# Kernel tuning notes

Hardware: AMD Instinct MI355X
Metric: run time of the kernel (lower is better)

The kernel has to match this reference:

```python
import jax, jax.numpy as jnp
import numpy as np

MAX_OBJECTS = 20
NODE_FEAT_DIM = 16
HID = 256
N_OPS = 8
N_COLORS = 10
B = 16384
EPS = 1e-5


def _ln(x, g, b):
    m = x.mean(-1, keepdims=True)
    v = ((x - m) ** 2).mean(-1, keepdims=True)
    return (x - m) / jnp.sqrt(v + EPS) * g + b


def _mlp(x, w1, b1, w2, b2):
    return jax.nn.relu(x @ w1 + b1) @ w2 + b2


def setup_inputs() -> dict:
    key = jax.random.key(0)
    ks = jax.random.split(key, 32)
    w = lambda k, shp: (jax.random.normal(k, shp, jnp.float32) * 0.02)
    return {
        "nf": jax.random.normal(ks[0], (B, MAX_OBJECTS, NODE_FEAT_DIM), jnp.float32),
        "nn_c": jax.random.randint(ks[1], (B,), 0, MAX_OBJECTS),
        "neW": w(ks[2], (NODE_FEAT_DIM, HID)), "neb": jnp.zeros((HID,), jnp.float32),
        "g1W1": w(ks[3], (2 * HID, HID)), "g1b1": jnp.zeros((HID,), jnp.float32),
        "g1W2": w(ks[4], (HID, HID)), "g1b2": jnp.zeros((HID,), jnp.float32),
        "g2W1": w(ks[5], (2 * HID, HID)), "g2b1": jnp.zeros((HID,), jnp.float32),
        "g2W2": w(ks[6], (HID, HID)), "g2b2": jnp.zeros((HID,), jnp.float32),
        "n1g": jnp.ones((HID,), jnp.float32), "n1b": jnp.zeros((HID,), jnp.float32),
        "n2g": jnp.ones((HID,), jnp.float32), "n2b": jnp.zeros((HID,), jnp.float32),
        "ohW": w(ks[7], (HID, N_OPS)), "ohb": jnp.zeros((N_OPS,), jnp.float32),
        "c1W": w(ks[8], (HID, N_COLORS)), "c1b": jnp.zeros((N_COLORS,), jnp.float32),
        "c2W": w(ks[9], (HID, N_COLORS)), "c2b": jnp.zeros((N_COLORS,), jnp.float32),
        "pqW": w(ks[10], (HID, HID)), "pqb": jnp.zeros((HID,), jnp.float32),
        "pkW": w(ks[11], (HID, HID)), "pkb": jnp.zeros((HID,), jnp.float32),
    }


def reference(nf, nn_c, neW, neb, g1W1, g1b1, g1W2, g1b2, g2W1, g2b1, g2W2, g2b2,
              n1g, n1b, n2g, n2b, ohW, ohb, c1W, c1b, c2W, c2b, pqW, pqb, pkW, pkb):
    mask = jnp.arange(MAX_OBJECTS)[None, :] < nn_c[:, None]  # [B, N]
    mf = mask.astype(jnp.float32)[..., None]                 # [B, N, 1]
    denom = jnp.clip(mf.sum(1, keepdims=True), 1.0)          # [B, 1, 1]

    h = nf @ neW + neb                                       # [B, N, H]
    msg = (h * mf).sum(1, keepdims=True) / denom             # [B, 1, H]
    h = h + _mlp(jnp.concatenate([h, jnp.broadcast_to(msg, h.shape)], -1), g1W1, g1b1, g1W2, g1b2)
    h = _ln(h, n1g, n1b) * mf

    msg = (h * mf).sum(1, keepdims=True) / denom
    h = h + _mlp(jnp.concatenate([h, jnp.broadcast_to(msg, h.shape)], -1), g2W1, g2b1, g2W2, g2b2)
    h = _ln(h, n2g, n2b) * mf

    g = (h * mf).sum(1) / jnp.clip(mf.sum(1), 1.0)           # [B, H]

    q = g @ pqW + pqb                                        # [B, H]
    k = h @ pkW + pkb                                        # [B, N, H]
    pl = jnp.einsum('bh,bnh->bn', q, k)
    pl = jnp.where(mask, pl, -1e9)
    return (g @ ohW + ohb, g @ c1W + c1b, g @ c2W + c2b, pl)
```

## Files before the change

kernel.cpp:

```cpp
#include <hip/hip_runtime.h>

typedef unsigned char u8;
typedef unsigned int  u32;
using f32x4 = __attribute__((ext_vector_type(4))) float;

#define DI __device__ __forceinline__

DI u32 pk4f8(float a, float b, float c, float d){
  int w = __builtin_amdgcn_cvt_pk_fp8_f32(a, b, 0, false);
  w = __builtin_amdgcn_cvt_pk_fp8_f32(c, d, w, true);
  return (u32)w;
}
DI u8 enc1(float a){
  return (u8)(__builtin_amdgcn_cvt_pk_fp8_f32(a, a, 0, false) & 0xFF);
}
DI float dc0(u32 v){ return __builtin_amdgcn_cvt_f32_fp8((int)v, 0); }
DI float dc1(u32 v){ return __builtin_amdgcn_cvt_f32_fp8((int)v, 1); }
DI float dc2(u32 v){ return __builtin_amdgcn_cvt_f32_fp8((int)v, 2); }
DI float dc3(u32 v){ return __builtin_amdgcn_cvt_f32_fp8((int)v, 3); }

DI f32x4 MFMA8(long a, long b, f32x4 c){
  return __builtin_amdgcn_mfma_f32_16x16x32_fp8_fp8(a, b, c, 0, 0, 0);
}

DI int swz8(int row, int col){ return (row << 8) + (col ^ ((row & 15) << 3)); }
DI long ldsA8(const u8* buf, int row, int k0){ return *(const long*)(buf + swz8(row, k0)); }
DI long ldG8(const u8* p){ return *(const long*)p; }

DI long mk8(float v0, float v1, float v2, float v3, float v4, float v5, float v6, float v7){
  u32 lo = pk4f8(v0, v1, v2, v3), hi = pk4f8(v4, v5, v6, v7);
  return (long)(((unsigned long long)hi << 32) | (unsigned long long)lo);
}
DI long loadW8T(const float* __restrict__ W, int n, int k0){
  return mk8(W[(k0+0)*256+n]*8.f, W[(k0+1)*256+n]*8.f, W[(k0+2)*256+n]*8.f, W[(k0+3)*256+n]*8.f,
             W[(k0+4)*256+n]*8.f, W[(k0+5)*256+n]*8.f, W[(k0+6)*256+n]*8.f, W[(k0+7)*256+n]*8.f);
}
DI long loadW8T16(const float* __restrict__ W, int n, int k0){
  float v[8];
#pragma unroll
  for (int j = 0; j < 8; j++){ int k = k0 + j; v[j] = (k < 16) ? W[k*256+n]*8.f : 0.f; }
  return mk8(v[0],v[1],v[2],v[3],v[4],v[5],v[6],v[7]);
}
DI long loadW8row(const float* __restrict__ W, int n, int k0){
  const float* p = W + n*256 + k0;
  return mk8(p[0]*8.f,p[1]*8.f,p[2]*8.f,p[3]*8.f,p[4]*8.f,p[5]*8.f,p[6]*8.f,p[7]*8.f);
}

#define WS_NEWT  0
#define WS_W1AT1 8192
#define WS_W1BT1 73728
#define WS_W2T1  139264
#define WS_W1AT2 204800
#define WS_W1BT2 270336
#define WS_W2T2  335872
#define WS_PQWT  401408
#define WS_PKWP  466944
#define WS_TOTAL 532480

__global__ void prep_weights(
    const float* __restrict__ neW, const float* __restrict__ g1W1,
    const float* __restrict__ g1W2, const float* __restrict__ g2W1,
    const float* __restrict__ g2W2, const float* __restrict__ pqW,
    const float* __restrict__ pkW, u8* __restrict__ ws)
{
  int i = blockIdx.x * 256 + threadIdx.x;
  if (i >= WS_TOTAL) return;
  float v;
  if (i < 8192){
    int n = i >> 5, k = i & 31;
    v = (k < 16) ? neW[k * 256 + n] : 0.0f;
  } else {
    int j = i - 8192;
    int region = j >> 16;
    int idx = j & 65535;
    int n = idx >> 8, k = idx & 255;
    switch (region){
      case 0: v = g1W1[k * 256 + n]; break;
      case 1: v = g1W1[(256 + k) * 256 + n]; break;
      case 2: v = g1W2[k * 256 + n]; break;
      case 3: v = g2W1[k * 256 + n]; break;
      case 4: v = g2W1[(256 + k) * 256 + n]; break;
      case 5: v = g2W2[k * 256 + n]; break;
      case 6: v = pqW[k * 256 + n]; break;
      default: v = pkW[idx]; break;
    }
  }
  ws[i] = enc1(v * 8.0f);
}

template<bool PREPPED>
__global__ __launch_bounds__(512, 2) void fused_graphnet(
    const float* __restrict__ nf, const int* __restrict__ nn_c,
    const float* __restrict__ neW, const float* __restrict__ neb,
    const float* __restrict__ g1W1, const float* __restrict__ g1b1,
    const float* __restrict__ g1W2, const float* __restrict__ g1b2,
    const float* __restrict__ g2W1, const float* __restrict__ g2b1,
    const float* __restrict__ g2W2, const float* __restrict__ g2b2,
    const float* __restrict__ n1g, const float* __restrict__ n1b,
    const float* __restrict__ n2g, const float* __restrict__ n2b,
    const float* __restrict__ ohW, const float* __restrict__ ohb,
    const float* __restrict__ c1W, const float* __restrict__ c1b,
    const float* __restrict__ c2W, const float* __restrict__ c2b,
    const float* __restrict__ pqW, const float* __restrict__ pqb,
    const float* __restrict__ pkW, const float* __restrict__ pkb,
    const u8* __restrict__ ws, float* __restrict__ out,
    int out_n, int Bv)
{
  __shared__ __align__(16) u8 bufA[80 * 256];
  __shared__ __align__(16) u8 bufB[80 * 256];
  __shared__ __align__(16) u8 smallA[8 * 256];
  __shared__ float pbf[4 * 256];
  __shared__ float rowstats[8][80][2];
  __shared__ float qdot[4];
  __shared__ int   cntS[4];
  __shared__ float dinvS[4];

  const int b0 = blockIdx.x * 4;
  const int tid = threadIdx.x;
  const int wave = tid >> 6, lane = tid & 63;
  const int lg = lane >> 4, lc = lane & 15;
  const int n0 = wave * 32;

  const int Bout = out_n / 48;
  const int off_c1 = 8 * Bout;
  const int off_c2 = 18 * Bout;
  const int off_pl = 28 * Bout;

  if (tid < 4){
    int bi = b0 + tid; if (bi >= Bv) bi = Bv - 1;
    int c = nn_c[bi];
    c = c < 0 ? 0 : (c > 20 ? 20 : c);
    cntS[tid] = c;
    dinvS[tid] = 1.0f / (float)(c < 1 ? 1 : c);
  }

  for (int i = tid; i < 80 * 4; i += 512){
    int row = i >> 2, c0 = 16 + (i & 3) * 4;
    *(u32*)(bufB + swz8(row, c0)) = 0u;
  }
  for (int i = tid; i < 80 * 4; i += 512){
    int row = i >> 2, k0 = (i & 3) * 4;
    int gr = b0 * 20 + row; if (gr >= Bv * 20) gr = Bv * 20 - 1;
    const float* p = nf + gr * 16 + k0;
    *(u32*)(bufB + swz8(row, k0)) = pk4f8(p[0], p[1], p[2], p[3]);
  }
  __syncthreads();

  const f32x4 zero4 = {0.0f, 0.0f, 0.0f, 0.0f};

  {
    long bw0, bw1;
    if constexpr (PREPPED){
      bw0 = ldG8(ws + WS_NEWT + (n0 + lc) * 32 + lg * 8);
      bw1 = ldG8(ws + WS_NEWT + (n0 + 16 + lc) * 32 + lg * 8);
    } else {
      bw0 = loadW8T16(neW, n0 + lc, lg * 8);
      bw1 = loadW8T16(neW, n0 + 16 + lc, lg * 8);
    }
    f32x4 acc[5][2];
#pragma unroll
    for (int mt = 0; mt < 5; mt++){
      long a = ldsA8(bufB, mt * 16 + lc, lg * 8);
      acc[mt][0] = MFMA8(a, bw0, zero4);
      acc[mt][1] = MFMA8(a, bw1, zero4);
    }
#pragma unroll
    for (int nt = 0; nt < 2; nt++){
      float bb = neb[n0 + nt * 16 + lc];
#pragma unroll
      for (int mt = 0; mt < 5; mt++)
#pragma unroll
        for (int r = 0; r < 4; r++){
          int row = mt * 16 + lg * 4 + r;
          int col = n0 + nt * 16 + lc;
          bufA[swz8(row, col)] = enc1(acc[mt][nt][r] * 0.125f + bb);
        }
    }
  }
  __syncthreads();

  for (int rd = 0; rd < 2; rd++){
    const int w1at = (rd == 0) ? WS_W1AT1 : WS_W1AT2;
    const int w1bt = (rd == 0) ? WS_W1BT1 : WS_W1BT2;
    const int w2t  = (rd == 0) ? WS_W2T1  : WS_W2T2;
    const float* W1 = (rd == 0) ? g1W1 : g2W1;
    const float* W2 = (rd == 0) ? g1W2 : g2W2;
    const float* b1p = (rd == 0) ? g1b1 : g2b1;
    const float* b2p = (rd == 0) ? g1b2 : g2b2;
    const float* ngp = (rd == 0) ? n1g : n2g;
    const float* nbp = (rd == 0) ? n1b : n2b;

    if (tid < 256){
      int b = tid >> 6;
      int c0 = (tid & 63) * 4;
      int c = cntS[b];
      float s0 = 0, s1 = 0, s2 = 0, s3 = 0;
      for (int r = 0; r < c; r++){
        u32 v = *(const u32*)(bufA + swz8(b * 20 + r, c0));
        s0 += dc0(v); s1 += dc1(v); s2 += dc2(v); s3 += dc3(v);
      }
      float di = dinvS[b];
      *(u32*)(smallA + swz8(b, c0)) = pk4f8(s0 * di, s1 * di, s2 * di, s3 * di);
    }
    __syncthreads();

    {
      long bw[16];
#pragma unroll
      for (int kk = 0; kk < 8; kk++){
        if constexpr (PREPPED){
          bw[kk * 2 + 0] = ldG8(ws + w1bt + (n0 + lc) * 256 + kk * 32 + lg * 8);
          bw[kk * 2 + 1] = ldG8(ws + w1bt + (n0 + 16 + lc) * 256 + kk * 32 + lg * 8);
        } else {
          bw[kk * 2 + 0] = loadW8T(W1 + 256 * 256, n0 + lc, kk * 32 + lg * 8);
          bw[kk * 2 + 1] = loadW8T(W1 + 256 * 256, n0 + 16 + lc, kk * 32 + lg * 8);
        }
      }
      f32x4 acc0 = zero4, acc1 = zero4;
#pragma unroll
      for (int kk = 0; kk < 8; kk++){
        long a = ldsA8(smallA, lc & 3, kk * 32 + lg * 8);
        acc0 = MFMA8(a, bw[kk * 2 + 0], acc0);
        acc1 = MFMA8(a, bw[kk * 2 + 1], acc1);
      }
      if (lg == 0){
#pragma unroll
        for (int r = 0; r < 4; r++){
          pbf[r * 256 + (n0 + lc)]      = acc0[r] * 0.125f + b1p[n0 + lc];
          pbf[r * 256 + (n0 + 16 + lc)] = acc1[r] * 0.125f + b1p[n0 + 16 + lc];
        }
      }
    }

    {
      long bw[16];
#pragma unroll
      for (int kk = 0; kk < 8; kk++){
        if constexpr (PREPPED){
          bw[kk * 2 + 0] = ldG8(ws + w1at + (n0 + lc) * 256 + kk * 32 + lg * 8);
          bw[kk * 2 + 1] = ldG8(ws + w1at + (n0 + 16 + lc) * 256 + kk * 32 + lg * 8);
        } else {
          bw[kk * 2 + 0] = loadW8T(W1, n0 + lc, kk * 32 + lg * 8);
          bw[kk * 2 + 1] = loadW8T(W1, n0 + 16 + lc, kk * 32 + lg * 8);
        }
      }
      f32x4 tacc[5][2];
#pragma unroll
      for (int mt = 0; mt < 5; mt++)
#pragma unroll
        for (int nt = 0; nt < 2; nt++) tacc[mt][nt] = zero4;
#pragma unroll
      for (int kk = 0; kk < 8; kk++){
#pragma unroll
        for (int mt = 0; mt < 5; mt++){
          long a = ldsA8(bufA, mt * 16 + lc, kk * 32 + lg * 8);
          tacc[mt][0] = MFMA8(a, bw[kk * 2 + 0], tacc[mt][0]);
          tacc[mt][1] = MFMA8(a, bw[kk * 2 + 1], tacc[mt][1]);
        }
      }
#pragma unroll
      for (int mt = 0; mt < 5; mt++)
#pragma unroll
        for (int nt = 0; nt < 2; nt++)
#pragma unroll
          for (int r = 0; r < 4; r++){
            int row = mt * 16 + lg * 4 + r;
            int col = n0 + nt * 16 + lc;
            float v = tacc[mt][nt][r] * 0.125f + pbf[(row / 20) * 256 + col];
            bufB[swz8(row, col)] = enc1(fmaxf(v, 0.0f));
          }
    }
    __syncthreads();

    {
      long bw[16];
#pragma unroll
      for (int kk = 0; kk < 8; kk++){
        if constexpr (PREPPED){
          bw[kk * 2 + 0] = ldG8(ws + w2t + (n0 + lc) * 256 + kk * 32 + lg * 8);
          bw[kk * 2 + 1] = ldG8(ws + w2t + (n0 + 16 + lc) * 256 + kk * 32 + lg * 8);
        } else {
          bw[kk * 2 + 0] = loadW8T(W2, n0 + lc, kk * 32 + lg * 8);
          bw[kk * 2 + 1] = loadW8T(W2, n0 + 16 + lc, kk * 32 + lg * 8);
        }
      }
      f32x4 tacc[5][2];
#pragma unroll
      for (int mt = 0; mt < 5; mt++)
#pragma unroll
        for (int nt = 0; nt < 2; nt++) tacc[mt][nt] = zero4;
#pragma unroll
      for (int kk = 0; kk < 8; kk++){
#pragma unroll
        for (int mt = 0; mt < 5; mt++){
          long a = ldsA8(bufB, mt * 16 + lc, kk * 32 + lg * 8);
          tacc[mt][0] = MFMA8(a, bw[kk * 2 + 0], tacc[mt][0]);
          tacc[mt][1] = MFMA8(a, bw[kk * 2 + 1], tacc[mt][1]);
        }
      }
#pragma unroll
      for (int nt = 0; nt < 2; nt++){
        float b2s = b2p[n0 + nt * 16 + lc];
#pragma unroll
        for (int mt = 0; mt < 5; mt++)
#pragma unroll
          for (int r = 0; r < 4; r++){
            int row = mt * 16 + lg * 4 + r;
            int col = n0 + nt * 16 + lc;
            u32 rv = bufA[swz8(row, col)];
            float v = tacc[mt][nt][r] * 0.125f + dc0(rv) + b2s;
            bufA[swz8(row, col)] = enc1(v);
          }
      }
    }

    {
#pragma unroll
      for (int mt = 0; mt < 5; mt++)
#pragma unroll
        for (int r = 0; r < 4; r++){
          int row = mt * 16 + lg * 4 + r;
          float s1 = 0, s2 = 0;
#pragma unroll
          for (int nt = 0; nt < 2; nt++){
            float v = dc0((u32)bufA[swz8(row, n0 + nt * 16 + lc)]);
            s1 += v; s2 += v * v;
          }
#pragma unroll
          for (int d = 1; d < 16; d <<= 1){ s1 += __shfl_xor(s1, d, 64); s2 += __shfl_xor(s2, d, 64); }
          if (lc == 0){ rowstats[wave][row][0] = s1; rowstats[wave][row][1] = s2; }
        }
      __syncthreads();

#pragma unroll
      for (int mt = 0; mt < 5; mt++)
#pragma unroll
        for (int r = 0; r < 4; r++){
          int row = mt * 16 + lg * 4 + r;
          float t1s = 0, t2s = 0;
#pragma unroll
          for (int w = 0; w < 8; w++){ t1s += rowstats[w][row][0]; t2s += rowstats[w][row][1]; }
          float mean = t1s * (1.0f / 256.0f);
          float var  = t2s * (1.0f / 256.0f) - mean * mean;
          float rstd = rsqrtf(fmaxf(var, 0.0f) + 1e-5f);
          int bb = row / 20;
          float mf = ((row - bb * 20) < cntS[bb]) ? 1.0f : 0.0f;
#pragma unroll
          for (int nt = 0; nt < 2; nt++){
            int col = n0 + nt * 16 + lc;
            float v = dc0((u32)bufA[swz8(row, col)]);
            bufA[swz8(row, col)] = enc1(((v - mean) * rstd * ngp[col] + nbp[col]) * mf);
          }
        }
    }
    __syncthreads();
  }

  if (tid < 256){
    int b = tid >> 6;
    int c0 = (tid & 63) * 4;
    int c = cntS[b];
    float s0 = 0, s1 = 0, s2 = 0, s3 = 0;
    for (int r = 0; r < c; r++){
      u32 v = *(const u32*)(bufA + swz8(b * 20 + r, c0));
      s0 += dc0(v); s1 += dc1(v); s2 += dc2(v); s3 += dc3(v);
    }
    float di = dinvS[b];
    *(u32*)(smallA + swz8(b, c0)) = pk4f8(s0 * di, s1 * di, s2 * di, s3 * di);
  }
  __syncthreads();

  {
    long bw[16];
#pragma unroll
    for (int kk = 0; kk < 8; kk++){
      if constexpr (PREPPED){
        bw[kk * 2 + 0] = ldG8(ws + WS_PQWT + (n0 + lc) * 256 + kk * 32 + lg * 8);
        bw[kk * 2 + 1] = ldG8(ws + WS_PQWT + (n0 + 16 + lc) * 256 + kk * 32 + lg * 8);
      } else {
        bw[kk * 2 + 0] = loadW8T(pqW, n0 + lc, kk * 32 + lg * 8);
        bw[kk * 2 + 1] = loadW8T(pqW, n0 + 16 + lc, kk * 32 + lg * 8);
      }
    }
    f32x4 qacc0 = zero4, qacc1 = zero4;
#pragma unroll
    for (int kk = 0; kk < 8; kk++){
      long a = ldsA8(smallA, lc & 3, kk * 32 + lg * 8);
      qacc0 = MFMA8(a, bw[kk * 2 + 0], qacc0);
      qacc1 = MFMA8(a, bw[kk * 2 + 1], qacc1);
    }
    if (lg == 0){
#pragma unroll
      for (int r = 0; r < 4; r++){
        smallA[swz8(4 + r, n0 + lc)]      = enc1(qacc0[r] * 0.125f + pqb[n0 + lc]);
        smallA[swz8(4 + r, n0 + 16 + lc)] = enc1(qacc1[r] * 0.125f + pqb[n0 + 16 + lc]);
      }
    }
  }
  __syncthreads();

  if (wave < 4){
    u32 qv = *(const u32*)(smallA + swz8(4 + wave, lane * 4));
    float p = dc0(qv) * pkb[lane * 4 + 0] + dc1(qv) * pkb[lane * 4 + 1]
            + dc2(qv) * pkb[lane * 4 + 2] + dc3(qv) * pkb[lane * 4 + 3];
#pragma unroll
    for (int d = 1; d < 64; d <<= 1) p += __shfl_xor(p, d, 64);
    if (lane == 0) qdot[wave] = p;
  }

  {
    long bw[16];
#pragma unroll
    for (int kk = 0; kk < 8; kk++){
      if constexpr (PREPPED){
        bw[kk * 2 + 0] = ldG8(ws + WS_PKWP + (n0 + lc) * 256 + kk * 32 + lg * 8);
        bw[kk * 2 + 1] = ldG8(ws + WS_PKWP + (n0 + 16 + lc) * 256 + kk * 32 + lg * 8);
      } else {
        bw[kk * 2 + 0] = loadW8row(pkW, n0 + lc, kk * 32 + lg * 8);
        bw[kk * 2 + 1] = loadW8row(pkW, n0 + 16 + lc, kk * 32 + lg * 8);
      }
    }
    f32x4 racc0 = zero4, racc1 = zero4;
#pragma unroll
    for (int kk = 0; kk < 8; kk++){
      long a = ldsA8(smallA, 4 + (lc & 3), kk * 32 + lg * 8);
      racc0 = MFMA8(a, bw[kk * 2 + 0], racc0);
      racc1 = MFMA8(a, bw[kk * 2 + 1], racc1);
    }
    if (lg == 0){
#pragma unroll
      for (int r = 0; r < 4; r++){
        pbf[r * 256 + (n0 + lc)]      = racc0[r] * 0.125f;
        pbf[r * 256 + (n0 + 16 + lc)] = racc1[r] * 0.125f;
      }
    }
  }
  __syncthreads();

  if (wave < 4){
    const int b = wave;
    if (b0 + b < Bv){
      int cb = cntS[b];
      float qd = qdot[b];
      for (int rr = 0; rr < 20; rr++){
        int row = b * 20 + rr;
        u32 hv = *(const u32*)(bufA + swz8(row, lane * 4));
        const float* rp = pbf + b * 256 + lane * 4;
        float p = dc0(hv) * rp[0] + dc1(hv) * rp[1] + dc2(hv) * rp[2] + dc3(hv) * rp[3];
#pragma unroll
        for (int d = 1; d < 64; d <<= 1) p += __shfl_xor(p, d, 64);
        if (lane == 0){
          float v = (rr < cb) ? (p + qd) : -1e9f;
          out[off_pl + (b0 + b) * 20 + rr] = v;
        }
      }
    }
  } else {
    const int b = wave - 4;
    if (b0 + b < Bv){
      u32 gv = *(const u32*)(smallA + swz8(b, lane * 4));
      float g0 = dc0(gv), g1 = dc1(gv), g2 = dc2(gv), g3 = dc3(gv);
#pragma unroll 1
      for (int o = 0; o < 28; o++){
        const float* W; const float* bias; int ncol, col, off;
        if (o < 8)      { W = ohW; bias = ohb; ncol = 8;  col = o;      off = 0; }
        else if (o < 18){ W = c1W; bias = c1b; ncol = 10; col = o - 8;  off = off_c1; }
        else            { W = c2W; bias = c2b; ncol = 10; col = o - 18; off = off_c2; }
        int k = lane * 4;
        float p = g0 * W[(k + 0) * ncol + col] + g1 * W[(k + 1) * ncol + col]
                + g2 * W[(k + 2) * ncol + col] + g3 * W[(k + 3) * ncol + col];
#pragma unroll
        for (int d = 1; d < 64; d <<= 1) p += __shfl_xor(p, d, 64);
        if (lane == 0) out[off + (b0 + b) * ncol + col] = p + bias[col];
      }
    }
  }
}

extern "C" void kernel_launch(void* const* d_in, const int* in_sizes, int n_in,
                              void* d_out, int out_size, void* d_ws, size_t ws_size,
                              hipStream_t stream)
{
  const float* nf   = (const float*)d_in[0];
  const int*   nn_c = (const int*)d_in[1];
  const float* neW  = (const float*)d_in[2];
  const float* neb  = (const float*)d_in[3];
  const float* g1W1 = (const float*)d_in[4];
  const float* g1b1 = (const float*)d_in[5];
  const float* g1W2 = (const float*)d_in[6];
  const float* g1b2 = (const float*)d_in[7];
  const float* g2W1 = (const float*)d_in[8];
  const float* g2b1 = (const float*)d_in[9];
  const float* g2W2 = (const float*)d_in[10];
  const float* g2b2 = (const float*)d_in[11];
  const float* n1g  = (const float*)d_in[12];
  const float* n1b  = (const float*)d_in[13];
  const float* n2g  = (const float*)d_in[14];
  const float* n2b  = (const float*)d_in[15];
  const float* ohW  = (const float*)d_in[16];
  const float* ohb  = (const float*)d_in[17];
  const float* c1W  = (const float*)d_in[18];
  const float* c1b  = (const float*)d_in[19];
  const float* c2W  = (const float*)d_in[20];
  const float* c2b  = (const float*)d_in[21];
  const float* pqW  = (const float*)d_in[22];
  const float* pqb  = (const float*)d_in[23];
  const float* pkW  = (const float*)d_in[24];
  const float* pkb  = (const float*)d_in[25];

  float* outp = (float*)d_out;
  u8* ws = (u8*)d_ws;
  int B = in_sizes[0] / 320;
  int grid = (B + 3) / 4;

  if (ws_size >= (size_t)WS_TOTAL){
    prep_weights<<<(WS_TOTAL + 255) / 256, 256, 0, stream>>>(
        neW, g1W1, g1W2, g2W1, g2W2, pqW, pkW, ws);
    fused_graphnet<true><<<grid, 512, 0, stream>>>(
        nf, nn_c, neW, neb, g1W1, g1b1, g1W2, g1b2, g2W1, g2b1, g2W2, g2b2,
        n1g, n1b, n2g, n2b, ohW, ohb, c1W, c1b, c2W, c2b, pqW, pqb, pkW, pkb,
        ws, outp, out_size, B);
  } else {
    fused_graphnet<false><<<grid, 512, 0, stream>>>(
        nf, nn_c, neW, neb, g1W1, g1b1, g1W2, g1b2, g2W1, g2b1, g2W2, g2b2,
        n1g, n1b, n2g, n2b, ohW, ohb, c1W, c1b, c2W, c2b, pqW, pqb, pkW, pkb,
        ws, outp, out_size, B);
  }
}
```

Before: 1.118 ms.

## Process eight graphs per 1024-thread block with two row halves sharing weight loads

```diff
diff --git a/kernel.cpp b/kernel.cpp
--- a/kernel.cpp
+++ b/kernel.cpp
@@ -89,7 +89,7 @@
 }
 
 template<bool PREPPED>
-__global__ __launch_bounds__(512, 2) void fused_graphnet(
+__global__ __launch_bounds__(1024, 2) void fused_graphnet(
     const float* __restrict__ nf, const int* __restrict__ nn_c,
     const float* __restrict__ neW, const float* __restrict__ neb,
     const float* __restrict__ g1W1, const float* __restrict__ g1b1,
@@ -106,27 +106,29 @@
     const u8* __restrict__ ws, float* __restrict__ out,
     int out_n, int Bv)
 {
-  __shared__ __align__(16) u8 bufA[80 * 256];
-  __shared__ __align__(16) u8 bufB[80 * 256];
-  __shared__ __align__(16) u8 smallA[8 * 256];
-  __shared__ float pbf[4 * 256];
-  __shared__ float rowstats[8][80][2];
-  __shared__ float qdot[4];
-  __shared__ int   cntS[4];
-  __shared__ float dinvS[4];
-
-  const int b0 = blockIdx.x * 4;
+  __shared__ __align__(16) u8 bufA[160 * 256];
+  __shared__ __align__(16) u8 bufB[160 * 256];
+  __shared__ __align__(16) u8 smallA[16 * 256];
+  __shared__ float pbf[8 * 256];
+  __shared__ float rowstats[8][160][2];
+  __shared__ float qdot[8];
+  __shared__ int   cntS[8];
+  __shared__ float dinvS[8];
+
+  const int b0 = blockIdx.x * 8;
   const int tid = threadIdx.x;
   const int wave = tid >> 6, lane = tid & 63;
   const int lg = lane >> 4, lc = lane & 15;
-  const int n0 = wave * 32;
+  const int rh = wave >> 3, cw = wave & 7;
+  const int n0 = cw * 32;
+  const int rb = rh * 80;
 
   const int Bout = out_n / 48;
   const int off_c1 = 8 * Bout;
   const int off_c2 = 18 * Bout;
   const int off_pl = 28 * Bout;
 
-  if (tid < 4){
+  if (tid < 8){
     int bi = b0 + tid; if (bi >= Bv) bi = Bv - 1;
     int c = nn_c[bi];
     c = c < 0 ? 0 : (c > 20 ? 20 : c);
@@ -134,12 +136,13 @@
     dinvS[tid] = 1.0f / (float)(c < 1 ? 1 : c);
   }
 
-  for (int i = tid; i < 80 * 4; i += 512){
-    int row = i >> 2, c0 = 16 + (i & 3) * 4;
+  if (tid < 16 * 64) *(u32*)(smallA + tid * 4) = 0u;
+  if (tid < 160 * 4){
+    int row = tid >> 2, c0 = 16 + (tid & 3) * 4;
     *(u32*)(bufB + swz8(row, c0)) = 0u;
   }
-  for (int i = tid; i < 80 * 4; i += 512){
-    int row = i >> 2, k0 = (i & 3) * 4;
+  if (tid < 160 * 4){
+    int row = tid >> 2, k0 = (tid & 3) * 4;
     int gr = b0 * 20 + row; if (gr >= Bv * 20) gr = Bv * 20 - 1;
     const float* p = nf + gr * 16 + k0;
     *(u32*)(bufB + swz8(row, k0)) = pk4f8(p[0], p[1], p[2], p[3]);
@@ -160,7 +163,7 @@
     f32x4 acc[5][2];
 #pragma unroll
     for (int mt = 0; mt < 5; mt++){
-      long a = ldsA8(bufB, mt * 16 + lc, lg * 8);
+      long a = ldsA8(bufB, rb + mt * 16 + lc, lg * 8);
       acc[mt][0] = MFMA8(a, bw0, zero4);
       acc[mt][1] = MFMA8(a, bw1, zero4);
     }
@@ -171,7 +174,7 @@
       for (int mt = 0; mt < 5; mt++)
 #pragma unroll
         for (int r = 0; r < 4; r++){
-          int row = mt * 16 + lg * 4 + r;
+          int row = rb + mt * 16 + lg * 4 + r;
           int col = n0 + nt * 16 + lc;
           bufA[swz8(row, col)] = enc1(acc[mt][nt][r] * 0.125f + bb);
         }
@@ -190,7 +193,7 @@
     const float* ngp = (rd == 0) ? n1g : n2g;
     const float* nbp = (rd == 0) ? n1b : n2b;
 
-    if (tid < 256){
+    if (tid < 512){
       int b = tid >> 6;
       int c0 = (tid & 63) * 4;
       int c = cntS[b];
@@ -219,15 +222,16 @@
       f32x4 acc0 = zero4, acc1 = zero4;
 #pragma unroll
       for (int kk = 0; kk < 8; kk++){
-        long a = ldsA8(smallA, lc & 3, kk * 32 + lg * 8);
+        long a = ldsA8(smallA, lc, kk * 32 + lg * 8);
         acc0 = MFMA8(a, bw[kk * 2 + 0], acc0);
         acc1 = MFMA8(a, bw[kk * 2 + 1], acc1);
       }
-      if (lg == 0){
+      if (rh == 0 && lg < 2){
 #pragma unroll
         for (int r = 0; r < 4; r++){
-          pbf[r * 256 + (n0 + lc)]      = acc0[r] * 0.125f + b1p[n0 + lc];
-          pbf[r * 256 + (n0 + 16 + lc)] = acc1[r] * 0.125f + b1p[n0 + 16 + lc];
+          int b = lg * 4 + r;
+          pbf[b * 256 + (n0 + lc)]      = acc0[r] * 0.125f + b1p[n0 + lc];
+          pbf[b * 256 + (n0 + 16 + lc)] = acc1[r] * 0.125f + b1p[n0 + 16 + lc];
         }
       }
     }
@@ -253,18 +257,19 @@
       for (int kk = 0; kk < 8; kk++){
 #pragma unroll
         for (int mt = 0; mt < 5; mt++){
-          long a = ldsA8(bufA, mt * 16 + lc, kk * 32 + lg * 8);
+          long a = ldsA8(bufA, rb + mt * 16 + lc, kk * 32 + lg * 8);
           tacc[mt][0] = MFMA8(a, bw[kk * 2 + 0], tacc[mt][0]);
           tacc[mt][1] = MFMA8(a, bw[kk * 2 + 1], tacc[mt][1]);
         }
       }
+      __syncthreads();
 #pragma unroll
       for (int mt = 0; mt < 5; mt++)
 #pragma unroll
         for (int nt = 0; nt < 2; nt++)
 #pragma unroll
           for (int r = 0; r < 4; r++){
-            int row = mt * 16 + lg * 4 + r;
+            int row = rb + mt * 16 + lg * 4 + r;
             int col = n0 + nt * 16 + lc;
             float v = tacc[mt][nt][r] * 0.125f + pbf[(row / 20) * 256 + col];
             bufB[swz8(row, col)] = enc1(fmaxf(v, 0.0f));
@@ -293,7 +298,7 @@
       for (int kk = 0; kk < 8; kk++){
 #pragma unroll
         for (int mt = 0; mt < 5; mt++){
-          long a = ldsA8(bufB, mt * 16 + lc, kk * 32 + lg * 8);
+          long a = ldsA8(bufB, rb + mt * 16 + lc, kk * 32 + lg * 8);
           tacc[mt][0] = MFMA8(a, bw[kk * 2 + 0], tacc[mt][0]);
           tacc[mt][1] = MFMA8(a, bw[kk * 2 + 1], tacc[mt][1]);
         }
@@ -305,7 +310,7 @@
         for (int mt = 0; mt < 5; mt++)
 #pragma unroll
           for (int r = 0; r < 4; r++){
-            int row = mt * 16 + lg * 4 + r;
+            int row = rb + mt * 16 + lg * 4 + r;
             int col = n0 + nt * 16 + lc;
             u32 rv = bufA[swz8(row, col)];
             float v = tacc[mt][nt][r] * 0.125f + dc0(rv) + b2s;
@@ -319,7 +324,7 @@
       for (int mt = 0; mt < 5; mt++)
 #pragma unroll
         for (int r = 0; r < 4; r++){
-          int row = mt * 16 + lg * 4 + r;
+          int row = rb + mt * 16 + lg * 4 + r;
           float s1 = 0, s2 = 0;
 #pragma unroll
           for (int nt = 0; nt < 2; nt++){
@@ -328,15 +333,21 @@
           }
 #pragma unroll
           for (int d = 1; d < 16; d <<= 1){ s1 += __shfl_xor(s1, d, 64); s2 += __shfl_xor(s2, d, 64); }
-          if (lc == 0){ rowstats[wave][row][0] = s1; rowstats[wave][row][1] = s2; }
+          if (lc == 0){ rowstats[cw][row][0] = s1; rowstats[cw][row][1] = s2; }
         }
       __syncthreads();
 
+      float ngv[2], nbv[2];
+#pragma unroll
+      for (int nt = 0; nt < 2; nt++){
+        ngv[nt] = ngp[n0 + nt * 16 + lc];
+        nbv[nt] = nbp[n0 + nt * 16 + lc];
+      }
 #pragma unroll
       for (int mt = 0; mt < 5; mt++)
 #pragma unroll
         for (int r = 0; r < 4; r++){
-          int row = mt * 16 + lg * 4 + r;
+          int row = rb + mt * 16 + lg * 4 + r;
           float t1s = 0, t2s = 0;
 #pragma unroll
           for (int w = 0; w < 8; w++){ t1s += rowstats[w][row][0]; t2s += rowstats[w][row][1]; }
@@ -349,14 +360,14 @@
           for (int nt = 0; nt < 2; nt++){
             int col = n0 + nt * 16 + lc;
             float v = dc0((u32)bufA[swz8(row, col)]);
-            bufA[swz8(row, col)] = enc1(((v - mean) * rstd * ngp[col] + nbp[col]) * mf);
+            bufA[swz8(row, col)] = enc1(((v - mean) * rstd * ngv[nt] + nbv[nt]) * mf);
           }
         }
     }
     __syncthreads();
   }
 
-  if (tid < 256){
+  if (tid < 512){
     int b = tid >> 6;
     int c0 = (tid & 63) * 4;
     int c = cntS[b];
@@ -385,22 +396,24 @@
     f32x4 qacc0 = zero4, qacc1 = zero4;
 #pragma unroll
     for (int kk = 0; kk < 8; kk++){
-      long a = ldsA8(smallA, lc & 3, kk * 32 + lg * 8);
+      long a = ldsA8(smallA, lc, kk * 32 + lg * 8);
       qacc0 = MFMA8(a, bw[kk * 2 + 0], qacc0);
       qacc1 = MFMA8(a, bw[kk * 2 + 1], qacc1);
     }
-    if (lg == 0){
+    __syncthreads();
+    if (rh == 0 && lg < 2){
 #pragma unroll
       for (int r = 0; r < 4; r++){
-        smallA[swz8(4 + r, n0 + lc)]      = enc1(qacc0[r] * 0.125f + pqb[n0 + lc]);
-        smallA[swz8(4 + r, n0 + 16 + lc)] = enc1(qacc1[r] * 0.125f + pqb[n0 + 16 + lc]);
+        int b = lg * 4 + r;
+        smallA[swz8(8 + b, n0 + lc)]      = enc1(qacc0[r] * 0.125f + pqb[n0 + lc]);
+        smallA[swz8(8 + b, n0 + 16 + lc)] = enc1(qacc1[r] * 0.125f + pqb[n0 + 16 + lc]);
       }
     }
   }
   __syncthreads();
 
-  if (wave < 4){
-    u32 qv = *(const u32*)(smallA + swz8(4 + wave, lane * 4));
+  if (wave < 8){
+    u32 qv = *(const u32*)(smallA + swz8(8 + wave, lane * 4));
     float p = dc0(qv) * pkb[lane * 4 + 0] + dc1(qv) * pkb[lane * 4 + 1]
             + dc2(qv) * pkb[lane * 4 + 2] + dc3(qv) * pkb[lane * 4 + 3];
 #pragma unroll
@@ -423,26 +436,28 @@
     f32x4 racc0 = zero4, racc1 = zero4;
 #pragma unroll
     for (int kk = 0; kk < 8; kk++){
-      long a = ldsA8(smallA, 4 + (lc & 3), kk * 32 + lg * 8);
+      long a = ldsA8(smallA, 8 + (lc & 7), kk * 32 + lg * 8);
       racc0 = MFMA8(a, bw[kk * 2 + 0], racc0);
       racc1 = MFMA8(a, bw[kk * 2 + 1], racc1);
     }
-    if (lg == 0){
+    if (rh == 0 && lg < 2){
 #pragma unroll
       for (int r = 0; r < 4; r++){
-        pbf[r * 256 + (n0 + lc)]      = racc0[r] * 0.125f;
-        pbf[r * 256 + (n0 + 16 + lc)] = racc1[r] * 0.125f;
+        int b = lg * 4 + r;
+        pbf[b * 256 + (n0 + lc)]      = racc0[r] * 0.125f;
+        pbf[b * 256 + (n0 + 16 + lc)] = racc1[r] * 0.125f;
       }
     }
   }
   __syncthreads();
 
-  if (wave < 4){
-    const int b = wave;
+  {
+    const int b = wave >> 1;
+    const int r0 = (wave & 1) * 10;
     if (b0 + b < Bv){
       int cb = cntS[b];
       float qd = qdot[b];
-      for (int rr = 0; rr < 20; rr++){
+      for (int rr = r0; rr < r0 + 10; rr++){
         int row = b * 20 + rr;
         u32 hv = *(const u32*)(bufA + swz8(row, lane * 4));
         const float* rp = pbf + b * 256 + lane * 4;
@@ -455,13 +470,16 @@
         }
       }
     }
-  } else {
-    const int b = wave - 4;
+  }
+
+  {
+    const int b = wave >> 1;
+    const int o0 = (wave & 1) * 14;
     if (b0 + b < Bv){
       u32 gv = *(const u32*)(smallA + swz8(b, lane * 4));
       float g0 = dc0(gv), g1 = dc1(gv), g2 = dc2(gv), g3 = dc3(gv);
 #pragma unroll 1
-      for (int o = 0; o < 28; o++){
+      for (int o = o0; o < o0 + 14; o++){
         const float* W; const float* bias; int ncol, col, off;
         if (o < 8)      { W = ohW; bias = ohb; ncol = 8;  col = o;      off = 0; }
         else if (o < 18){ W = c1W; bias = c1b; ncol = 10; col = o - 8;  off = off_c1; }
@@ -511,17 +529,17 @@
   float* outp = (float*)d_out;
   u8* ws = (u8*)d_ws;
   int B = in_sizes[0] / 320;
-  int grid = (B + 3) / 4;
+  int grid = (B + 7) / 8;
 
   if (ws_size >= (size_t)WS_TOTAL){
     prep_weights<<<(WS_TOTAL + 255) / 256, 256, 0, stream>>>(
         neW, g1W1, g1W2, g2W1, g2W2, pqW, pkW, ws);
-    fused_graphnet<true><<<grid, 512, 0, stream>>>(
+    fused_graphnet<true><<<grid, 1024, 0, stream>>>(
         nf, nn_c, neW, neb, g1W1, g1b1, g1W2, g1b2, g2W1, g2b1, g2W2, g2b2,
         n1g, n1b, n2g, n2b, ohW, ohb, c1W, c1b, c2W, c2b, pqW, pqb, pkW, pkb,
         ws, outp, out_size, B);
   } else {
-    fused_graphnet<false><<<grid, 512, 0, stream>>>(
+    fused_graphnet<false><<<grid, 1024, 0, stream>>>(
         nf, nn_c, neW, neb, g1W1, g1b1, g1W2, g1b2, g2W1, g2b1, g2W2, g2b2,
         n1g, n1b, n2g, n2b, ohW, ohb, c1W, c1b, c2W, c2b, pqW, pqb, pkW, pkb,
         ws, outp, out_size, B);
```

After: 1.792 ms. +60.3%, slower.

## Shrink block to 256 threads with each wave covering 64 columns in two halves

Applied to the files above, without the earlier changes.

```diff
diff --git a/kernel.cpp b/kernel.cpp
--- a/kernel.cpp
+++ b/kernel.cpp
@@ -89,7 +89,7 @@
 }
 
 template<bool PREPPED>
-__global__ __launch_bounds__(512, 2) void fused_graphnet(
+__global__ __launch_bounds__(256, 3) void fused_graphnet(
     const float* __restrict__ nf, const int* __restrict__ nn_c,
     const float* __restrict__ neW, const float* __restrict__ neb,
     const float* __restrict__ g1W1, const float* __restrict__ g1b1,
@@ -110,7 +110,7 @@
   __shared__ __align__(16) u8 bufB[80 * 256];
   __shared__ __align__(16) u8 smallA[8 * 256];
   __shared__ float pbf[4 * 256];
-  __shared__ float rowstats[8][80][2];
+  __shared__ float rowstats[4][80][2];
   __shared__ float qdot[4];
   __shared__ int   cntS[4];
   __shared__ float dinvS[4];
@@ -119,7 +119,7 @@
   const int tid = threadIdx.x;
   const int wave = tid >> 6, lane = tid & 63;
   const int lg = lane >> 4, lc = lane & 15;
-  const int n0 = wave * 32;
+  const int n0 = wave * 64;
 
   const int Bout = out_n / 48;
   const int off_c1 = 8 * Bout;
@@ -134,11 +134,11 @@
     dinvS[tid] = 1.0f / (float)(c < 1 ? 1 : c);
   }
 
-  for (int i = tid; i < 80 * 4; i += 512){
+  for (int i = tid; i < 80 * 4; i += 256){
     int row = i >> 2, c0 = 16 + (i & 3) * 4;
     *(u32*)(bufB + swz8(row, c0)) = 0u;
   }
-  for (int i = tid; i < 80 * 4; i += 512){
+  for (int i = tid; i < 80 * 4; i += 256){
     int row = i >> 2, k0 = (i & 3) * 4;
     int gr = b0 * 20 + row; if (gr >= Bv * 20) gr = Bv * 20 - 1;
     const float* p = nf + gr * 16 + k0;
@@ -148,14 +148,16 @@
 
   const f32x4 zero4 = {0.0f, 0.0f, 0.0f, 0.0f};
 
-  {
+#pragma unroll 1
+  for (int nh = 0; nh < 2; nh++){
+    const int n0h = n0 + nh * 32;
     long bw0, bw1;
     if constexpr (PREPPED){
-      bw0 = ldG8(ws + WS_NEWT + (n0 + lc) * 32 + lg * 8);
-      bw1 = ldG8(ws + WS_NEWT + (n0 + 16 + lc) * 32 + lg * 8);
+      bw0 = ldG8(ws + WS_NEWT + (n0h + lc) * 32 + lg * 8);
+      bw1 = ldG8(ws + WS_NEWT + (n0h + 16 + lc) * 32 + lg * 8);
     } else {
-      bw0 = loadW8T16(neW, n0 + lc, lg * 8);
-      bw1 = loadW8T16(neW, n0 + 16 + lc, lg * 8);
+      bw0 = loadW8T16(neW, n0h + lc, lg * 8);
+      bw1 = loadW8T16(neW, n0h + 16 + lc, lg * 8);
     }
     f32x4 acc[5][2];
 #pragma unroll
@@ -166,14 +168,13 @@
     }
 #pragma unroll
     for (int nt = 0; nt < 2; nt++){
-      float bb = neb[n0 + nt * 16 + lc];
+      float bb = neb[n0h + nt * 16 + lc];
 #pragma unroll
       for (int mt = 0; mt < 5; mt++)
 #pragma unroll
         for (int r = 0; r < 4; r++){
           int row = mt * 16 + lg * 4 + r;
-          int col = n0 + nt * 16 + lc;
-          bufA[swz8(row, col)] = enc1(acc[mt][nt][r] * 0.125f + bb);
+          bufA[swz8(row, n0h + nt * 16 + lc)] = enc1(acc[mt][nt][r] * 0.125f + bb);
         }
     }
   }
@@ -190,7 +191,7 @@
     const float* ngp = (rd == 0) ? n1g : n2g;
     const float* nbp = (rd == 0) ? n1b : n2b;
 
-    if (tid < 256){
+    {
       int b = tid >> 6;
       int c0 = (tid & 63) * 4;
       int c = cntS[b];
@@ -204,16 +205,18 @@
     }
     __syncthreads();
 
-    {
+#pragma unroll 1
+    for (int nh = 0; nh < 2; nh++){
+      const int n0h = n0 + nh * 32;
       long bw[16];
 #pragma unroll
       for (int kk = 0; kk < 8; kk++){
         if constexpr (PREPPED){
-          bw[kk * 2 + 0] = ldG8(ws + w1bt + (n0 + lc) * 256 + kk * 32 + lg * 8);
-          bw[kk * 2 + 1] = ldG8(ws + w1bt + (n0 + 16 + lc) * 256 + kk * 32 + lg * 8);
+          bw[kk * 2 + 0] = ldG8(ws + w1bt + (n0h + lc) * 256 + kk * 32 + lg * 8);
+          bw[kk * 2 + 1] = ldG8(ws + w1bt + (n0h + 16 + lc) * 256 + kk * 32 + lg * 8);
         } else {
-          bw[kk * 2 + 0] = loadW8T(W1 + 256 * 256, n0 + lc, kk * 32 + lg * 8);
-          bw[kk * 2 + 1] = loadW8T(W1 + 256 * 256, n0 + 16 + lc, kk * 32 + lg * 8);
+          bw[kk * 2 + 0] = loadW8T(W1 + 256 * 256, n0h + lc, kk * 32 + lg * 8);
+          bw[kk * 2 + 1] = loadW8T(W1 + 256 * 256, n0h + 16 + lc, kk * 32 + lg * 8);
         }
       }
       f32x4 acc0 = zero4, acc1 = zero4;
@@ -226,29 +229,29 @@
       if (lg == 0){
 #pragma unroll
         for (int r = 0; r < 4; r++){
-          pbf[r * 256 + (n0 + lc)]      = acc0[r] * 0.125f + b1p[n0 + lc];
-          pbf[r * 256 + (n0 + 16 + lc)] = acc1[r] * 0.125f + b1p[n0 + 16 + lc];
-        }
-      }
-    }
-
-    {
+          pbf[r * 256 + (n0h + lc)]      = acc0[r] * 0.125f + b1p[n0h + lc];
+          pbf[r * 256 + (n0h + 16 + lc)] = acc1[r] * 0.125f + b1p[n0h + 16 + lc];
+        }
+      }
+    }
+
+#pragma unroll 1
+    for (int nh = 0; nh < 2; nh++){
+      const int n0h = n0 + nh * 32;
       long bw[16];
 #pragma unroll
       for (int kk = 0; kk < 8; kk++){
         if constexpr (PREPPED){
-          bw[kk * 2 + 0] = ldG8(ws + w1at + (n0 + lc) * 256 + kk * 32 + lg * 8);
-          bw[kk * 2 + 1] = ldG8(ws + w1at + (n0 + 16 + lc) * 256 + kk * 32 + lg * 8);
+          bw[kk * 2 + 0] = ldG8(ws + w1at + (n0h + lc) * 256 + kk * 32 + lg * 8);
+          bw[kk * 2 + 1] = ldG8(ws + w1at + (n0h + 16 + lc) * 256 + kk * 32 + lg * 8);
         } else {
-          bw[kk * 2 + 0] = loadW8T(W1, n0 + lc, kk * 32 + lg * 8);
-          bw[kk * 2 + 1] = loadW8T(W1, n0 + 16 + lc, kk * 32 + lg * 8);
+          bw[kk * 2 + 0] = loadW8T(W1, n0h + lc, kk * 32 + lg * 8);
+          bw[kk * 2 + 1] = loadW8T(W1, n0h + 16 + lc, kk * 32 + lg * 8);
         }
       }
       f32x4 tacc[5][2];
 #pragma unroll
-      for (int mt = 0; mt < 5; mt++)
-#pragma unroll
-        for (int nt = 0; nt < 2; nt++) tacc[mt][nt] = zero4;
+      for (int mt = 0; mt < 5; mt++){ tacc[mt][0] = zero4; tacc[mt][1] = zero4; }
 #pragma unroll
       for (int kk = 0; kk < 8; kk++){
 #pragma unroll
@@ -265,30 +268,30 @@
 #pragma unroll
           for (int r = 0; r < 4; r++){
             int row = mt * 16 + lg * 4 + r;
-            int col = n0 + nt * 16 + lc;
+            int col = n0h + nt * 16 + lc;
             float v = tacc[mt][nt][r] * 0.125f + pbf[(row / 20) * 256 + col];
             bufB[swz8(row, col)] = enc1(fmaxf(v, 0.0f));
           }
     }
     __syncthreads();
 
-    {
+#pragma unroll 1
+    for (int nh = 0; nh < 2; nh++){
+      const int n0h = n0 + nh * 32;
       long bw[16];
 #pragma unroll
       for (int kk = 0; kk < 8; kk++){
         if constexpr (PREPPED){
-          bw[kk * 2 + 0] = ldG8(ws + w2t + (n0 + lc) * 256 + kk * 32 + lg * 8);
-          bw[kk * 2 + 1] = ldG8(ws + w2t + (n0 + 16 + lc) * 256 + kk * 32 + lg * 8);
+          bw[kk * 2 + 0] = ldG8(ws + w2t + (n0h + lc) * 256 + kk * 32 + lg * 8);
+          bw[kk * 2 + 1] = ldG8(ws + w2t + (n0h + 16 + lc) * 256 + kk * 32 + lg * 8);
         } else {
-          bw[kk * 2 + 0] = loadW8T(W2, n0 + lc, kk * 32 + lg * 8);
-          bw[kk * 2 + 1] = loadW8T(W2, n0 + 16 + lc, kk * 32 + lg * 8);
+          bw[kk * 2 + 0] = loadW8T(W2, n0h + lc, kk * 32 + lg * 8);
+          bw[kk * 2 + 1] = loadW8T(W2, n0h + 16 + lc, kk * 32 + lg * 8);
         }
       }
       f32x4 tacc[5][2];
 #pragma unroll
-      for (int mt = 0; mt < 5; mt++)
-#pragma unroll
-        for (int nt = 0; nt < 2; nt++) tacc[mt][nt] = zero4;
+      for (int mt = 0; mt < 5; mt++){ tacc[mt][0] = zero4; tacc[mt][1] = zero4; }
 #pragma unroll
       for (int kk = 0; kk < 8; kk++){
 #pragma unroll
@@ -300,13 +303,13 @@
       }
 #pragma unroll
       for (int nt = 0; nt < 2; nt++){
-        float b2s = b2p[n0 + nt * 16 + lc];
+        float b2s = b2p[n0h + nt * 16 + lc];
 #pragma unroll
         for (int mt = 0; mt < 5; mt++)
 #pragma unroll
           for (int r = 0; r < 4; r++){
             int row = mt * 16 + lg * 4 + r;
-            int col = n0 + nt * 16 + lc;
+            int col = n0h + nt * 16 + lc;
             u32 rv = bufA[swz8(row, col)];
             float v = tacc[mt][nt][r] * 0.125f + dc0(rv) + b2s;
             bufA[swz8(row, col)] = enc1(v);
@@ -322,7 +325,7 @@
           int row = mt * 16 + lg * 4 + r;
           float s1 = 0, s2 = 0;
 #pragma unroll
-          for (int nt = 0; nt < 2; nt++){
+          for (int nt = 0; nt < 4; nt++){
             float v = dc0((u32)bufA[swz8(row, n0 + nt * 16 + lc)]);
             s1 += v; s2 += v * v;
           }
@@ -337,16 +340,15 @@
 #pragma unroll
         for (int r = 0; r < 4; r++){
           int row = mt * 16 + lg * 4 + r;
-          float t1s = 0, t2s = 0;
-#pragma unroll
-          for (int w = 0; w < 8; w++){ t1s += rowstats[w][row][0]; t2s += rowstats[w][row][1]; }
+          float t1s = rowstats[0][row][0] + rowstats[1][row][0] + rowstats[2][row][0] + rowstats[3][row][0];
+          float t2s = rowstats[0][row][1] + rowstats[1][row][1] + rowstats[2][row][1] + rowstats[3][row][1];
           float mean = t1s * (1.0f / 256.0f);
           float var  = t2s * (1.0f / 256.0f) - mean * mean;
           float rstd = rsqrtf(fmaxf(var, 0.0f) + 1e-5f);
           int bb = row / 20;
           float mf = ((row - bb * 20) < cntS[bb]) ? 1.0f : 0.0f;
 #pragma unroll
-          for (int nt = 0; nt < 2; nt++){
+          for (int nt = 0; nt < 4; nt++){
             int col = n0 + nt * 16 + lc;
             float v = dc0((u32)bufA[swz8(row, col)]);
             bufA[swz8(row, col)] = enc1(((v - mean) * rstd * ngp[col] + nbp[col]) * mf);
@@ -356,7 +358,7 @@
     __syncthreads();
   }
 
-  if (tid < 256){
+  {
     int b = tid >> 6;
     int c0 = (tid & 63) * 4;
     int c = cntS[b];
@@ -370,16 +372,18 @@
   }
   __syncthreads();
 
-  {
+#pragma unroll 1
+  for (int nh = 0; nh < 2; nh++){
+    const int n0h = n0 + nh * 32;
     long bw[16];
 #pragma unroll
     for (int kk = 0; kk < 8; kk++){
       if constexpr (PREPPED){
-        bw[kk * 2 + 0] = ldG8(ws + WS_PQWT + (n0 + lc) * 256 + kk * 32 + lg * 8);
-        bw[kk * 2 + 1] = ldG8(ws + WS_PQWT + (n0 + 16 + lc) * 256 + kk * 32 + lg * 8);
+        bw[kk * 2 + 0] = ldG8(ws + WS_PQWT + (n0h + lc) * 256 + kk * 32 + lg * 8);
+        bw[kk * 2 + 1] = ldG8(ws + WS_PQWT + (n0h + 16 + lc) * 256 + kk * 32 + lg * 8);
       } else {
-        bw[kk * 2 + 0] = loadW8T(pqW, n0 + lc, kk * 32 + lg * 8);
-        bw[kk * 2 + 1] = loadW8T(pqW, n0 + 16 + lc, kk * 32 + lg * 8);
+        bw[kk * 2 + 0] = loadW8T(pqW, n0h + lc, kk * 32 + lg * 8);
+        bw[kk * 2 + 1] = loadW8T(pqW, n0h + 16 + lc, kk * 32 + lg * 8);
       }
     }
     f32x4 qacc0 = zero4, qacc1 = zero4;
@@ -392,14 +396,14 @@
     if (lg == 0){
 #pragma unroll
       for (int r = 0; r < 4; r++){
-        smallA[swz8(4 + r, n0 + lc)]      = enc1(qacc0[r] * 0.125f + pqb[n0 + lc]);
-        smallA[swz8(4 + r, n0 + 16 + lc)] = enc1(qacc1[r] * 0.125f + pqb[n0 + 16 + lc]);
+        smallA[swz8(4 + r, n0h + lc)]      = enc1(qacc0[r] * 0.125f + pqb[n0h + lc]);
+        smallA[swz8(4 + r, n0h + 16 + lc)] = enc1(qacc1[r] * 0.125f + pqb[n0h + 16 + lc]);
       }
     }
   }
   __syncthreads();
 
-  if (wave < 4){
+  {
     u32 qv = *(const u32*)(smallA + swz8(4 + wave, lane * 4));
     float p = dc0(qv) * pkb[lane * 4 + 0] + dc1(qv) * pkb[lane * 4 + 1]
             + dc2(qv) * pkb[lane * 4 + 2] + dc3(qv) * pkb[lane * 4 + 3];
@@ -408,16 +412,18 @@
     if (lane == 0) qdot[wave] = p;
   }
 
-  {
+#pragma unroll 1
+  for (int nh = 0; nh < 2; nh++){
+    const int n0h = n0 + nh * 32;
     long bw[16];
 #pragma unroll
     for (int kk = 0; kk < 8; kk++){
       if constexpr (PREPPED){
-        bw[kk * 2 + 0] = ldG8(ws + WS_PKWP + (n0 + lc) * 256 + kk * 32 + lg * 8);
-        bw[kk * 2 + 1] = ldG8(ws + WS_PKWP + (n0 + 16 + lc) * 256 + kk * 32 + lg * 8);
+        bw[kk * 2 + 0] = ldG8(ws + WS_PKWP + (n0h + lc) * 256 + kk * 32 + lg * 8);
+        bw[kk * 2 + 1] = ldG8(ws + WS_PKWP + (n0h + 16 + lc) * 256 + kk * 32 + lg * 8);
       } else {
-        bw[kk * 2 + 0] = loadW8row(pkW, n0 + lc, kk * 32 + lg * 8);
-        bw[kk * 2 + 1] = loadW8row(pkW, n0 + 16 + lc, kk * 32 + lg * 8);
+        bw[kk * 2 + 0] = loadW8row(pkW, n0h + lc, kk * 32 + lg * 8);
+        bw[kk * 2 + 1] = loadW8row(pkW, n0h + 16 + lc, kk * 32 + lg * 8);
       }
     }
     f32x4 racc0 = zero4, racc1 = zero4;
@@ -430,14 +436,14 @@
     if (lg == 0){
 #pragma unroll
       for (int r = 0; r < 4; r++){
-        pbf[r * 256 + (n0 + lc)]      = racc0[r] * 0.125f;
-        pbf[r * 256 + (n0 + 16 + lc)] = racc1[r] * 0.125f;
+        pbf[r * 256 + (n0h + lc)]      = racc0[r] * 0.125f;
+        pbf[r * 256 + (n0h + 16 + lc)] = racc1[r] * 0.125f;
       }
     }
   }
   __syncthreads();
 
-  if (wave < 4){
+  {
     const int b = wave;
     if (b0 + b < Bv){
       int cb = cntS[b];
@@ -455,8 +461,10 @@
         }
       }
     }
-  } else {
-    const int b = wave - 4;
+  }
+
+  {
+    const int b = wave;
     if (b0 + b < Bv){
       u32 gv = *(const u32*)(smallA + swz8(b, lane * 4));
       float g0 = dc0(gv), g1 = dc1(gv), g2 = dc2(gv), g3 = dc3(gv);
@@ -516,12 +524,12 @@
   if (ws_size >= (size_t)WS_TOTAL){
     prep_weights<<<(WS_TOTAL + 255) / 256, 256, 0, stream>>>(
         neW, g1W1, g1W2, g2W1, g2W2, pqW, pkW, ws);
-    fused_graphnet<true><<<grid, 512, 0, stream>>>(
+    fused_graphnet<true><<<grid, 256, 0, stream>>>(
         nf, nn_c, neW, neb, g1W1, g1b1, g1W2, g1b2, g2W1, g2b1, g2W2, g2b2,
         n1g, n1b, n2g, n2b, ohW, ohb, c1W, c1b, c2W, c2b, pqW, pqb, pkW, pkb,
         ws, outp, out_size, B);
   } else {
-    fused_graphnet<false><<<grid, 512, 0, stream>>>(
+    fused_graphnet<false><<<grid, 256, 0, stream>>>(
         nf, nn_c, neW, neb, g1W1, g1b1, g1W2, g1b2, g2W1, g2b1, g2W2, g2b2,
         n1g, n1b, n2g, n2b, ohW, ohb, c1W, c1b, c2W, c2b, pqW, pqb, pkW, pkb,
         ws, outp, out_size, B);
```

Measured after the change: 1.149 ms. +2.8%, slower.
